# Performance work log

Measured on AMD Instinct MI355X. Metric: run time of the kernel, lower is better.

The kernel has to match this reference:

```python
import jax, jax.numpy as jnp
import numpy as np

N_GAUSS = 16  # matches init_kwargs n_gaussians


def _so3_forward(z, n):
    # z: [B, 6n]. First 3n entries -> axis params, rest -> logvar logits.
    v = z[:, :3 * n].reshape(-1, n, 3)
    a, b, c = v[..., 0], v[..., 1], v[..., 2]
    zero = jnp.zeros_like(a)
    # antisym_matrix: A = [[0, a, b], [-a, 0, c], [-b, -c, 0]]  (skew-symmetric)
    A = jnp.stack([
        jnp.stack([zero, a, b], axis=-1),
        jnp.stack([-a, zero, c], axis=-1),
        jnp.stack([-b, -c, zero], axis=-1),
    ], axis=-2)  # [B, n, 3, 3]
    # matrix_exp of a skew-symmetric 3x3 == Rodrigues formula (exact):
    # exp(A) = I + sin(t)/t * A + (1-cos(t))/t^2 * A^2, t = ||(a,b,c)||
    th2 = a * a + b * b + c * c
    small = th2 < 1e-8
    t2 = jnp.where(small, jnp.ones_like(th2), th2)  # safe denom
    t = jnp.sqrt(t2)
    s1 = jnp.where(small, 1.0 - th2 / 6.0, jnp.sin(t) / t)
    s2 = jnp.where(small, 0.5 - th2 / 24.0, (1.0 - jnp.cos(t)) / t2)
    A2 = A @ A  # [B, n, 3, 3]
    I = jnp.eye(3, dtype=z.dtype)
    mean = I + s1[..., None, None] * A + s2[..., None, None] * A2
    logvar = 5.4 * jax.nn.sigmoid(z[:, 3 * n:].reshape(-1, n, 3)) - 9.2
    return mean, logvar


def setup_inputs() -> dict:
    key = jax.random.key(0)
    B = 262144
    z = jax.random.normal(key, (B, 6 * N_GAUSS), dtype=jnp.float32)
    return {"z": z}


def reference(z):
    return _so3_forward(z, N_GAUSS)
```

## Files before the change

kernel.cpp:

```cpp
#include <hip/hip_runtime.h>


#define BLOCK 256

typedef float f4 __attribute__((ext_vector_type(4)));

__global__ __launch_bounds__(BLOCK, 8) void so3_encode_kernel(
    const float* __restrict__ z,
    float* __restrict__ out_mean,
    float* __restrict__ out_logvar)
{
    __shared__ float smean[4][64 * 9];
    __shared__ float slv[4][64 * 3];

    const int t    = threadIdx.x;
    const int lane = t & 63;
    const int w    = t >> 6;
    const int g    = blockIdx.x * BLOCK + t;
    const int b    = g >> 4;
    const int s    = g & 15;

    const float* zr = z + (size_t)b * 96 + s * 3;
    float a  = zr[0];
    float bb = zr[1];
    float c  = zr[2];
    float x0 = zr[48];
    float x1 = zr[49];
    float x2 = zr[50];

    float th2 = a * a + bb * bb + c * c;
    bool small = th2 < 1e-8f;
    float t2 = small ? 1.0f : th2;
    float tt = sqrtf(t2);
    float sn, cs;
    __sincosf(tt, &sn, &cs);
    float inv_t2 = 1.0f / t2;
    float s1 = small ? (1.0f - th2 * (1.0f / 6.0f))  : (sn * tt * inv_t2);
    float s2 = small ? (0.5f - th2 * (1.0f / 24.0f)) : ((1.0f - cs) * inv_t2);

    float ab = a * bb, ac = a * c, bc = bb * c;
    float* sm = &smean[w][lane * 9];
    sm[0] = 1.0f - s2 * (a * a + bb * bb);
    sm[1] = s1 * a  - s2 * bc;
    sm[2] = s1 * bb + s2 * ac;
    sm[3] = -s1 * a - s2 * bc;
    sm[4] = 1.0f - s2 * (a * a + c * c);
    sm[5] = s1 * c  - s2 * ab;
    sm[6] = -s1 * bb + s2 * ac;
    sm[7] = -s1 * c  - s2 * ab;
    sm[8] = 1.0f - s2 * (bb * bb + c * c);

    float* sl = &slv[w][lane * 3];
    sl[0] = 5.4f / (1.0f + __expf(-x0)) - 9.2f;
    sl[1] = 5.4f / (1.0f + __expf(-x1)) - 9.2f;
    sl[2] = 5.4f / (1.0f + __expf(-x2)) - 9.2f;

    asm volatile("s_waitcnt lgkmcnt(0)" ::: "memory");
    __builtin_amdgcn_sched_barrier(0);

    const int g_base = blockIdx.x * BLOCK + (w << 6);

    const f4* smv = reinterpret_cast<const f4*>(&smean[w][0]);
    f4* om = reinterpret_cast<f4*>(out_mean + (size_t)g_base * 9);
    om[lane]      = smv[lane];
    om[64 + lane] = smv[64 + lane];
    if (lane < 16) om[128 + lane] = smv[128 + lane];

    const f4* slvv = reinterpret_cast<const f4*>(&slv[w][0]);
    f4* ol = reinterpret_cast<f4*>(out_logvar + (size_t)g_base * 3);
    if (lane < 48) ol[lane] = slvv[lane];
}

extern "C" void kernel_launch(void* const* d_in, const int* in_sizes, int n_in,
                              void* d_out, int out_size, void* d_ws, size_t ws_size,
                              hipStream_t stream) {
    const float* z = (const float*)d_in[0];
    const int B = in_sizes[0] / 96;
    float* out_mean = (float*)d_out;
    float* out_logvar = (float*)d_out + (size_t)B * 16 * 9;

    const int nthreads = B * 16;
    const int grid = nthreads / BLOCK;
    so3_encode_kernel<<<grid, BLOCK, 0, stream>>>(z, out_mean, out_logvar);
}
```

Before: 51.62 us.

## Map threads to output float4s and drop the LDS staging buffer

Each thread now produces one float4 of the packed output directly instead of one gaussian per thread. Mean-region threads recompute the Rodrigues matrix for up to two gaussians and select four consecutive elements with a switch, and logvar threads apply the sigmoid to a vectorized float4 load. This removes the shared-memory transpose and the partially idle lanes in the stores. In exchange it recomputes the trig work about twice per gaussian, adds integer divides, and introduces divergent switch selection.

```diff
diff --git a/kernel.cpp b/kernel.cpp
--- a/kernel.cpp
+++ b/kernel.cpp
@@ -5,70 +5,81 @@
 
 typedef float f4 __attribute__((ext_vector_type(4)));
 
+struct M9 { float e0, e1, e2, e3, e4, e5, e6, e7, e8; };
+
+__device__ __forceinline__ M9 rodrigues(float a, float b, float c) {
+    float th2 = a * a + b * b + c * c;
+    bool small = th2 < 1e-8f;
+    float t2 = small ? 1.0f : th2;
+    float t = sqrtf(t2);
+    float sn, cs;
+    __sincosf(t, &sn, &cs);
+    float inv = 1.0f / t2;
+    float s1 = small ? (1.0f - th2 * (1.0f / 6.0f))  : (sn * t * inv);
+    float s2 = small ? (0.5f - th2 * (1.0f / 24.0f)) : ((1.0f - cs) * inv);
+    float ab = a * b, ac = a * c, bc = b * c;
+    M9 m;
+    m.e0 = 1.0f - s2 * (a * a + b * b);
+    m.e1 = s1 * a - s2 * bc;
+    m.e2 = s1 * b + s2 * ac;
+    m.e3 = -s1 * a - s2 * bc;
+    m.e4 = 1.0f - s2 * (a * a + c * c);
+    m.e5 = s1 * c - s2 * ab;
+    m.e6 = -s1 * b + s2 * ac;
+    m.e7 = -s1 * c - s2 * ab;
+    m.e8 = 1.0f - s2 * (b * b + c * c);
+    return m;
+}
+
 __global__ __launch_bounds__(BLOCK, 8) void so3_encode_kernel(
     const float* __restrict__ z,
-    float* __restrict__ out_mean,
-    float* __restrict__ out_logvar)
+    float* __restrict__ out,
+    unsigned M4,
+    unsigned NG)
 {
-    __shared__ float smean[4][64 * 9];
-    __shared__ float slv[4][64 * 3];
+    const unsigned q = blockIdx.x * BLOCK + threadIdx.x;
+    f4* outv = reinterpret_cast<f4*>(out);
 
-    const int t    = threadIdx.x;
-    const int lane = t & 63;
-    const int w    = t >> 6;
-    const int g    = blockIdx.x * BLOCK + t;
-    const int b    = g >> 4;
-    const int s    = g & 15;
+    if (q < M4) {
+        unsigned j0 = 4u * q;
+        unsigned g0 = j0 / 9u;
+        unsigned r  = j0 - 9u * g0;
+        unsigned g1 = g0 + 1u;
+        if (g1 >= NG) g1 = NG - 1u;
 
-    const float* zr = z + (size_t)b * 96 + s * 3;
-    float a  = zr[0];
-    float bb = zr[1];
-    float c  = zr[2];
-    float x0 = zr[48];
-    float x1 = zr[49];
-    float x2 = zr[50];
+        unsigned a0 = (g0 >> 4) * 96u + (g0 & 15u) * 3u;
+        unsigned a1 = (g1 >> 4) * 96u + (g1 & 15u) * 3u;
+        const float* p0 = z + a0;
+        const float* p1 = z + a1;
+        M9 m0 = rodrigues(p0[0], p0[1], p0[2]);
+        M9 m1 = rodrigues(p1[0], p1[1], p1[2]);
 
-    float th2 = a * a + bb * bb + c * c;
-    bool small = th2 < 1e-8f;
-    float t2 = small ? 1.0f : th2;
-    float tt = sqrtf(t2);
-    float sn, cs;
-    __sincosf(tt, &sn, &cs);
-    float inv_t2 = 1.0f / t2;
-    float s1 = small ? (1.0f - th2 * (1.0f / 6.0f))  : (sn * tt * inv_t2);
-    float s2 = small ? (0.5f - th2 * (1.0f / 24.0f)) : ((1.0f - cs) * inv_t2);
-
-    float ab = a * bb, ac = a * c, bc = bb * c;
-    float* sm = &smean[w][lane * 9];
-    sm[0] = 1.0f - s2 * (a * a + bb * bb);
-    sm[1] = s1 * a  - s2 * bc;
-    sm[2] = s1 * bb + s2 * ac;
-    sm[3] = -s1 * a - s2 * bc;
-    sm[4] = 1.0f - s2 * (a * a + c * c);
-    sm[5] = s1 * c  - s2 * ab;
-    sm[6] = -s1 * bb + s2 * ac;
-    sm[7] = -s1 * c  - s2 * ab;
-    sm[8] = 1.0f - s2 * (bb * bb + c * c);
-
-    float* sl = &slv[w][lane * 3];
-    sl[0] = 5.4f / (1.0f + __expf(-x0)) - 9.2f;
-    sl[1] = 5.4f / (1.0f + __expf(-x1)) - 9.2f;
-    sl[2] = 5.4f / (1.0f + __expf(-x2)) - 9.2f;
-
-    asm volatile("s_waitcnt lgkmcnt(0)" ::: "memory");
-    __builtin_amdgcn_sched_barrier(0);
-
-    const int g_base = blockIdx.x * BLOCK + (w << 6);
-
-    const f4* smv = reinterpret_cast<const f4*>(&smean[w][0]);
-    f4* om = reinterpret_cast<f4*>(out_mean + (size_t)g_base * 9);
-    om[lane]      = smv[lane];
-    om[64 + lane] = smv[64 + lane];
-    if (lane < 16) om[128 + lane] = smv[128 + lane];
-
-    const f4* slvv = reinterpret_cast<const f4*>(&slv[w][0]);
-    f4* ol = reinterpret_cast<f4*>(out_logvar + (size_t)g_base * 3);
-    if (lane < 48) ol[lane] = slvv[lane];
+        f4 o;
+        switch (r) {
+            case 0: o.x = m0.e0; o.y = m0.e1; o.z = m0.e2; o.w = m0.e3; break;
+            case 1: o.x = m0.e1; o.y = m0.e2; o.z = m0.e3; o.w = m0.e4; break;
+            case 2: o.x = m0.e2; o.y = m0.e3; o.z = m0.e4; o.w = m0.e5; break;
+            case 3: o.x = m0.e3; o.y = m0.e4; o.z = m0.e5; o.w = m0.e6; break;
+            case 4: o.x = m0.e4; o.y = m0.e5; o.z = m0.e6; o.w = m0.e7; break;
+            case 5: o.x = m0.e5; o.y = m0.e6; o.z = m0.e7; o.w = m0.e8; break;
+            case 6: o.x = m0.e6; o.y = m0.e7; o.z = m0.e8; o.w = m1.e0; break;
+            case 7: o.x = m0.e7; o.y = m0.e8; o.z = m1.e0; o.w = m1.e1; break;
+            default: o.x = m0.e8; o.y = m1.e0; o.z = m1.e1; o.w = m1.e2; break;
+        }
+        outv[q] = o;
+    } else {
+        unsigned u   = q - M4;
+        unsigned row = u / 12u;
+        unsigned col = u - 12u * row;
+        const f4* src = reinterpret_cast<const f4*>(z + (size_t)row * 96 + 48) + col;
+        f4 v = *src;
+        f4 o;
+        o.x = 5.4f / (1.0f + __expf(-v.x)) - 9.2f;
+        o.y = 5.4f / (1.0f + __expf(-v.y)) - 9.2f;
+        o.z = 5.4f / (1.0f + __expf(-v.z)) - 9.2f;
+        o.w = 5.4f / (1.0f + __expf(-v.w)) - 9.2f;
+        outv[q] = o;
+    }
 }
 
 extern "C" void kernel_launch(void* const* d_in, const int* in_sizes, int n_in,
@@ -76,10 +87,11 @@
                               hipStream_t stream) {
     const float* z = (const float*)d_in[0];
     const int B = in_sizes[0] / 96;
-    float* out_mean = (float*)d_out;
-    float* out_logvar = (float*)d_out + (size_t)B * 16 * 9;
+    const unsigned M4 = (unsigned)B * 36u;
+    const unsigned L4 = (unsigned)B * 12u;
+    const unsigned NG = (unsigned)B * 16u;
 
-    const int nthreads = B * 16;
-    const int grid = nthreads / BLOCK;
-    so3_encode_kernel<<<grid, BLOCK, 0, stream>>>(z, out_mean, out_logvar);
+    const unsigned total = M4 + L4;
+    const unsigned grid = (total + BLOCK - 1) / BLOCK;
+    so3_encode_kernel<<<grid, BLOCK, 0, stream>>>(z, (float*)d_out, M4, NG);
 }
```

Result: slower. 84.01 us (+62.8%).
